# Kernel tuning notes

Hardware: AMD Instinct MI355X
Metric: run time of the kernel (lower is better)

Reference implementation:

```python
import jax, jax.numpy as jnp
import numpy as np

X = 512; Y = 512; C = 3; NK = 15
DT = 0.2; DD = 2; SIGMA = 0.95
THETA_X = 2.0; N_EXP = 2.0
K_SIZE = 16

# mesh-grid positions, cell centers at +0.5 (matches construct_mesh_grid)
POS = (jnp.stack(jnp.meshgrid(jnp.arange(X), jnp.arange(Y), indexing='ij'), axis=-1) + 0.5).astype(jnp.float32)  # [X,Y,2]


def _dwconv(img, k):
    # img [X,Y,C'] -> depthwise 3x3 cross-correlation with 'same' zero padding (matches torch conv2d)
    z = img.transpose(2, 0, 1)[None]                      # [1,C',X,Y]
    kern = jnp.tile(k[None, None], (z.shape[1], 1, 1, 1))  # [C',1,3,3]
    out = jax.lax.conv_general_dilated(z, kern, (1, 1), 'SAME', feature_group_count=z.shape[1])
    return out[0].transpose(1, 2, 0)


def _sobel(img):
    # returns [X,Y,2,C'] with (sy, sx) stacked on axis 2, matching torch code order
    kx = jnp.array([[-1., 0., 1.], [-2., 0., 2.], [-1., 0., 1.]], jnp.float32)
    return jnp.stack([_dwconv(img, kx.T), _dwconv(img, kx)], axis=2)


def _reintegrate(grid, F):
    # Flow-Lenia reintegration tracking: 25 static roll offsets, fused accumulation
    ma = DD - SIGMA
    mu = POS[..., None] + jnp.clip(DT * F, -ma, ma)  # [X,Y,2,C]
    mu = jnp.clip(mu, SIGMA, X - SIGMA)
    clip_hi = min(1.0, 2.0 * SIGMA)
    inv_area = 1.0 / (4.0 * SIGMA ** 2)
    acc = jnp.zeros_like(grid)
    for dx in range(-DD, DD + 1):
        for dy in range(-DD, DD + 1):
            gridR = jnp.roll(grid, (dx, dy), (0, 1))
            muR = jnp.roll(mu, (dx, dy), (0, 1))
            sz = 0.5 - jnp.abs(POS[..., None] - muR) + SIGMA
            area = jnp.prod(jnp.clip(sz, 0.0, clip_hi), axis=2) * inv_area  # [X,Y,C]
            acc = acc + gridR * area
    return acc


def _forward(x, Ks, m, s, h, w_c1, c0):
    # spectral kernels: normalize, fftshift, fft2 (matches construct_kernels)
    Ksn = Ks / Ks.sum(axis=(0, 1), keepdims=True)
    fk = jnp.fft.fft2(jnp.fft.fftshift(Ksn, axes=(0, 1)), axes=(0, 1))  # [X,Y,NK] complex
    fXs = jnp.fft.fft2(x, axes=(0, 1))
    Us = jnp.fft.ifft2(fk * fXs[:, :, c0], axes=(0, 1)).real            # [X,Y,NK]
    # growth * h (note: h appears again inside w_c1, faithful to original double multiply)
    Gs = (jnp.exp(-(((Us - m) / s) ** 2) * 0.5) * 2.0 - 1.0) * h
    Hs = jnp.einsum('xyk,kc->xyc', Gs, w_c1)                             # [X,Y,C]
    grad_u = _sobel(Hs)                                                  # [X,Y,2,C]
    grad_x = _sobel(x.sum(-1, keepdims=True))                            # [X,Y,2,1]
    alpha = jnp.clip((x[:, :, None, :] / THETA_X) ** N_EXP, 0.0, 1.0)    # [X,Y,1,C]
    F = grad_u * (1.0 - alpha) - grad_x * alpha                          # [X,Y,2,C]
    return _reintegrate(x, F)


def setup_inputs() -> dict:
    key = jax.random.key(0)
    k1, k2, k3, k4, k5 = jax.random.split(key, 5)
    x = jax.random.uniform(k1, (X, Y, C), jnp.float32)
    # ring kernels per construct_kernels (non-sparse branch)
    mg = np.mgrid[-X // 2:X // 2, -Y // 2:Y // 2]
    base = np.linalg.norm(mg, axis=0).astype(np.float32)
    ks_list = []
    for i in range(NK):
        r = 0.6 + 0.04 * i
        D = base / ((K_SIZE + 15) * r)
        sig = 0.5 * (np.tanh(-(D - 1.0) * 10.0 / 2.0) + 1.0)
        bell = np.exp(-(D - 0.5) ** 2 / 0.15)
        ks_list.append(sig * bell)
    Ks = jnp.asarray(np.stack(ks_list, -1).astype(np.float32))
    m = 0.1 + 0.3 * jax.random.uniform(k2, (NK,), jnp.float32)
    s = 0.03 + 0.15 * jax.random.uniform(k3, (NK,), jnp.float32)
    h = 0.3 + 0.7 * jax.random.uniform(k4, (NK,), jnp.float32)
    c0 = jax.random.randint(k5, (NK,), 0, C, jnp.int32)
    c1 = jnp.arange(NK) % C
    w_c1 = jax.nn.one_hot(c1, C, dtype=jnp.float32) * h[:, None]
    return {"x": x, "Ks": Ks, "m": m, "s": s, "h": h, "w_c1": w_c1, "c0": c0}


def reference(x, Ks, m, s, h, w_c1, c0):
    return _forward(x, Ks, m, s, h, w_c1, c0)
```

## Files before the change

### kernel.cpp

```cpp
#include <hip/hip_runtime.h>
#include <math.h>

#define NPIX 262144
#define NKER 15
#define PI_F 3.14159265358979323846f
#define HW 264
#define CS 578
#define SK(n) ((n) + ((n) >> 3))

__device__ __forceinline__ float2 cadd(float2 a, float2 b) { return make_float2(a.x + b.x, a.y + b.y); }
__device__ __forceinline__ float2 csub(float2 a, float2 b) { return make_float2(a.x - b.x, a.y - b.y); }
__device__ __forceinline__ float2 cmul(float2 a, float2 b) {
  return make_float2(a.x * b.x - a.y * b.y, a.x * b.y + a.y * b.x);
}

__device__ __forceinline__ void fft_roots(int lane, float2* w1, float2* wh) {
  float s, c;
  sincosf(-2.0f * PI_F * (float)lane / 512.0f, &s, &c);
  *w1 = make_float2(c, s);
  int h = lane & ~7;
  *wh = make_float2(__shfl(c, h, 64), __shfl(s, h, 64));
}

template <bool INV>
__device__ __forceinline__ void dft8(float2 a[8]) {
  const float R = 0.70710678118654752f;
  float2 t0 = cadd(a[0], a[4]), u0 = csub(a[0], a[4]);
  float2 t1 = cadd(a[1], a[5]), u1 = csub(a[1], a[5]);
  float2 t2 = cadd(a[2], a[6]), u2 = csub(a[2], a[6]);
  float2 t3 = cadd(a[3], a[7]), u3 = csub(a[3], a[7]);
  u1 = INV ? make_float2(R * (u1.x - u1.y), R * (u1.x + u1.y))
           : make_float2(R * (u1.x + u1.y), R * (u1.y - u1.x));
  u2 = INV ? make_float2(-u2.y, u2.x) : make_float2(u2.y, -u2.x);
  u3 = INV ? make_float2(-R * (u3.x + u3.y), R * (u3.x - u3.y))
           : make_float2(R * (u3.y - u3.x), -R * (u3.x + u3.y));
  float2 e0 = cadd(t0, t2), f0 = csub(t0, t2);
  float2 e1 = cadd(t1, t3), f1 = csub(t1, t3);
  f1 = INV ? make_float2(-f1.y, f1.x) : make_float2(f1.y, -f1.x);
  float2 g0 = cadd(u0, u2), h0 = csub(u0, u2);
  float2 g1 = cadd(u1, u3), h1 = csub(u1, u3);
  h1 = INV ? make_float2(-h1.y, h1.x) : make_float2(h1.y, -h1.x);
  a[0] = cadd(e0, e1); a[4] = csub(e0, e1);
  a[2] = cadd(f0, f1); a[6] = csub(f0, f1);
  a[1] = cadd(g0, g1); a[5] = csub(g0, g1);
  a[3] = cadd(h0, h1); a[7] = csub(h0, h1);
}

template <bool INV>
__device__ __forceinline__ void fft512_r8(float2 a[8], float2* buf, int lane,
                                          float2 w1, float2 wh) {
  float2 wa = INV ? make_float2(w1.x, -w1.y) : w1;
  float2 wb = INV ? make_float2(wh.x, -wh.y) : wh;
  dft8<INV>(a);
  {
    float2 tq = wa;
    a[1] = cmul(a[1], tq);
#pragma unroll
    for (int q = 2; q < 8; ++q) { tq = cmul(tq, wa); a[q] = cmul(a[q], tq); }
  }
#pragma unroll
  for (int q = 0; q < 8; ++q) buf[9 * lane + q] = a[q];
#pragma unroll
  for (int q = 0; q < 8; ++q) a[q] = buf[SK(lane + 64 * q)];
  dft8<INV>(a);
  {
    float2 tq = wb;
    a[1] = cmul(a[1], tq);
#pragma unroll
    for (int q = 2; q < 8; ++q) { tq = cmul(tq, wb); a[q] = cmul(a[q], tq); }
  }
  int h = lane & ~7;
  int b2 = 9 * h + (lane - h);
#pragma unroll
  for (int q = 0; q < 8; ++q) buf[b2 + 9 * q] = a[q];
#pragma unroll
  for (int q = 0; q < 8; ++q) a[q] = buf[SK(lane + 64 * q)];
  dft8<INV>(a);
}

__device__ __forceinline__ void split_store_halfplane(float2 a[8], float2* buf, int lane,
                                                      float2* d0, float2* d1) {
#pragma unroll
  for (int q = 0; q < 8; ++q) buf[SK(lane + 64 * q)] = a[q];
#pragma unroll
  for (int q = 0; q < 4; ++q) {
    int v = lane + 64 * q;
    int mir = (512 - v) & 511;
    float2 P = a[q];
    float2 Qc = buf[SK(mir)];
    float2 Q = make_float2(Qc.x, -Qc.y);
    d0[v] = make_float2(0.5f * (P.x + Q.x), 0.5f * (P.y + Q.y));
    d1[v] = make_float2(0.5f * (P.y - Q.y), -0.5f * (P.x - Q.x));
  }
  if (lane == 0) {
    float2 P = a[4];
    d0[256] = make_float2(P.x, 0.f);
    d1[256] = make_float2(P.y, 0.f);
  }
}

__global__ void prep_rows(const float* __restrict__ Ks, const float* __restrict__ x,
                          float* __restrict__ Kt, float* __restrict__ partial,
                          float2* __restrict__ AxH) {
  __shared__ float wsum[4][16];
  __shared__ float2 scr[4][CS];
  int t = threadIdx.x, wave = t >> 6, lane = t & 63;
  if (blockIdx.x < 1024) {
    int p = blockIdx.x * 256 + t;
    const float* src = Ks + (size_t)p * NKER;
    float v[NKER];
#pragma unroll
    for (int k = 0; k < NKER; ++k) v[k] = src[k];
#pragma unroll
    for (int k = 0; k < NKER; ++k) Kt[(size_t)k * NPIX + p] = v[k];
#pragma unroll
    for (int k = 0; k < NKER; ++k) {
#pragma unroll
      for (int off = 32; off > 0; off >>= 1) v[k] += __shfl_down(v[k], off, 64);
    }
    if ((t & 63) == 0) {
#pragma unroll
      for (int k = 0; k < NKER; ++k) wsum[wave][k] = v[k];
    }
    __syncthreads();
    if (t < NKER)
      partial[blockIdx.x * 16 + t] = wsum[0][t] + wsum[1][t] + wsum[2][t] + wsum[3][t];
  } else {
    int b = blockIdx.x - 1024;
    int c = b >> 6;
    int rp = (b & 63) * 4 + wave;
    int r0 = rp, r1 = rp + 256;
    float2 w1, wh;
    fft_roots(lane, &w1, &wh);
    float2 a[8];
#pragma unroll
    for (int q = 0; q < 8; ++q) {
      int y = lane + 64 * q;
      a[q] = make_float2(x[((size_t)r0 * 512 + y) * 3 + c],
                         x[((size_t)r1 * 512 + y) * 3 + c]);
    }
    fft512_r8<false>(a, &scr[wave][0], lane, w1, wh);
    float2* d0 = AxH + ((size_t)c * 512 + r0) * HW;
    float2* d1 = AxH + ((size_t)c * 512 + r1) * HW;
    split_store_halfplane(a, &scr[wave][0], lane, d0, d1);
  }
}

__global__ void fft_rows_k(const float* __restrict__ Kt, float2* __restrict__ AkH) {
  __shared__ float2 scr[4][CS];
  int t = threadIdx.x, wave = t >> 6, lane = t & 63;
  int rp = blockIdx.x * 4 + wave;
  int k = blockIdx.y;
  const float* s0 = Kt + (size_t)k * NPIX + (size_t)(rp + 256) * 512;
  const float* s1 = Kt + (size_t)k * NPIX + (size_t)rp * 512;
  float2 w1, wh;
  fft_roots(lane, &w1, &wh);
  float2 a[8];
#pragma unroll
  for (int q = 0; q < 8; ++q) {
    int ys = (lane + 64 * q + 256) & 511;
    a[q] = make_float2(s0[ys], s1[ys]);
  }
  fft512_r8<false>(a, &scr[wave][0], lane, w1, wh);
  float2* d0 = AkH + ((size_t)k * 512 + rp) * HW;
  float2* d1 = AkH + ((size_t)k * 512 + rp + 256) * HW;
  split_store_halfplane(a, &scr[wave][0], lane, d0, d1);
}

__global__ void cols_x(const float2* __restrict__ AxH, float2* __restrict__ XH,
                       const float* __restrict__ partial, float* __restrict__ sums) {
  __shared__ float2 buf[8 * CS];
  __shared__ float red[512];
  int t = threadIdx.x;
  if (blockIdx.x == 33) {
    if (blockIdx.y != 0) return;
    int k = t & 15, g = t >> 4;
    float acc = 0.f;
    for (int b = g; b < 1024; b += 32) acc += partial[b * 16 + k];
    red[t] = acc;
    __syncthreads();
    if (t < 16) {
      float s = 0.f;
#pragma unroll
      for (int g2 = 0; g2 < 32; ++g2) s += red[g2 * 16 + t];
      sums[t] = s;
    }
    return;
  }
  int col0 = blockIdx.x * 8, ch = blockIdx.y;
  int c = t >> 6, lane = t & 63;
  float2 w1, wh;
  fft_roots(lane, &w1, &wh);
  const float2* bx = AxH + (size_t)ch * 512 * HW;
  float2* dst = XH + (size_t)ch * 512 * HW;
#pragma unroll
  for (int u = 0; u < 8; ++u) {
    int idx = (u << 9) + t;
    int row = idx >> 3, cc = idx & 7;
    buf[cc * CS + SK(row)] = bx[(size_t)row * HW + col0 + cc];
  }
  __syncthreads();
  float2 a[8];
#pragma unroll
  for (int q = 0; q < 8; ++q) a[q] = buf[c * CS + SK(lane + 64 * q)];
  fft512_r8<false>(a, &buf[c * CS], lane, w1, wh);
#pragma unroll
  for (int q = 0; q < 8; ++q) buf[c * CS + SK(lane + 64 * q)] = a[q];
  __syncthreads();
#pragma unroll
  for (int u = 0; u < 8; ++u) {
    int idx = (u << 9) + t;
    int row = idx >> 3, cc = idx & 7;
    dst[(size_t)row * HW + col0 + cc] = buf[cc * CS + SK(row)];
  }
}

__global__ void fused_cols(float2* __restrict__ AkH, const float2* __restrict__ XH,
                           const int* __restrict__ c0) {
  __shared__ float2 buf[8 * CS];
  int t = threadIdx.x, col0 = blockIdx.x * 8, k = blockIdx.y;
  int c = t >> 6, lane = t & 63;
  float2 w1, wh;
  fft_roots(lane, &w1, &wh);
  const float2* bx = XH + (size_t)c0[k] * 512 * HW;
  float2* bk = AkH + (size_t)k * 512 * HW;
  int col = col0 + c;
  float2 xh[8];
#pragma unroll
  for (int q = 0; q < 8; ++q) xh[q] = bx[(size_t)(lane + 64 * q) * HW + col];
#pragma unroll
  for (int u = 0; u < 8; ++u) {
    int idx = (u << 9) + t;
    int row = idx >> 3, cc = idx & 7;
    buf[cc * CS + SK(row)] = bk[(size_t)row * HW + col0 + cc];
  }
  __syncthreads();
  float2 a[8];
#pragma unroll
  for (int q = 0; q < 8; ++q) a[q] = buf[c * CS + SK(lane + 64 * q)];
  fft512_r8<false>(a, &buf[c * CS], lane, w1, wh);
#pragma unroll
  for (int q = 0; q < 8; ++q) a[q] = cmul(a[q], xh[q]);
  fft512_r8<true>(a, &buf[c * CS], lane, w1, wh);
#pragma unroll
  for (int q = 0; q < 8; ++q) buf[c * CS + SK(lane + 64 * q)] = a[q];
  __syncthreads();
#pragma unroll
  for (int u = 0; u < 8; ++u) {
    int idx = (u << 9) + t;
    int row = idx >> 3, cc = idx & 7;
    bk[(size_t)row * HW + col0 + cc] = buf[cc * CS + SK(row)];
  }
}

__global__ void irows_growth_combine(const float2* __restrict__ AkH,
                                     const float* __restrict__ sums,
                                     const float* __restrict__ m, const float* __restrict__ s,
                                     const float* __restrict__ h, const float* __restrict__ w,
                                     float* __restrict__ Hs) {
  __shared__ float2 scr[4][CS];
  __shared__ float accL[4][3][512];
  __shared__ float mk[16], isk[16], hk[16], wk[16][3], sck[16];
  int t = threadIdx.x, wave = t >> 6, lane = t & 63;
  int row = blockIdx.x;
  if (t < NKER) {
    mk[t] = m[t]; isk[t] = 1.0f / s[t]; hk[t] = h[t];
    sck[t] = 1.0f / (sums[t] * 262144.0f);
    wk[t][0] = w[t * 3 + 0]; wk[t][1] = w[t * 3 + 1]; wk[t][2] = w[t * 3 + 2];
  }
  __syncthreads();
  float2 w1, wh;
  fft_roots(lane, &w1, &wh);
  float acc[3][8];
#pragma unroll
  for (int cc = 0; cc < 3; ++cc)
#pragma unroll
    for (int q = 0; q < 8; ++q) acc[cc][q] = 0.f;
  for (int si = 0; si < 2; ++si) {
    int slot = wave + 4 * si;
    int k1 = 2 * slot, k2 = 2 * slot + 1;
    bool dual = (k2 < NKER);
    const float2* p1 = AkH + ((size_t)k1 * 512 + row) * HW;
    const float2* p2 = AkH + ((size_t)(dual ? k2 : k1) * 512 + row) * HW;
    float2 a[8];
#pragma unroll
    for (int q = 0; q < 8; ++q) {
      int v = lane + 64 * q;
      if (v <= 256) {
        float2 A1 = p1[v];
        float2 A2 = dual ? p2[v] : make_float2(0.f, 0.f);
        a[q] = make_float2(A1.x - A2.y, A1.y + A2.x);
      } else {
        int mi = 512 - v;
        float2 A1 = p1[mi];
        float2 A2 = dual ? p2[mi] : make_float2(0.f, 0.f);
        a[q] = make_float2(A1.x + A2.y, -A1.y + A2.x);
      }
    }
    fft512_r8<true>(a, &scr[wave][0], lane, w1, wh);
    float m1 = mk[k1], i1 = isk[k1], h1 = hk[k1], s1 = sck[k1];
    float w10 = wk[k1][0], w11 = wk[k1][1], w12 = wk[k1][2];
#pragma unroll
    for (int q = 0; q < 8; ++q) {
      float tt = (a[q].x * s1 - m1) * i1;
      float g = (expf(-0.5f * tt * tt) * 2.0f - 1.0f) * h1;
      acc[0][q] += g * w10; acc[1][q] += g * w11; acc[2][q] += g * w12;
    }
    if (dual) {
      float m2 = mk[k2], i2 = isk[k2], h2 = hk[k2], s2 = sck[k2];
      float w20 = wk[k2][0], w21 = wk[k2][1], w22 = wk[k2][2];
#pragma unroll
      for (int q = 0; q < 8; ++q) {
        float tt = (a[q].y * s2 - m2) * i2;
        float g = (expf(-0.5f * tt * tt) * 2.0f - 1.0f) * h2;
        acc[0][q] += g * w20; acc[1][q] += g * w21; acc[2][q] += g * w22;
      }
    }
  }
#pragma unroll
  for (int cc = 0; cc < 3; ++cc)
#pragma unroll
    for (int q = 0; q < 8; ++q) accL[wave][cc][lane + 64 * q] = acc[cc][q];
  __syncthreads();
#pragma unroll
  for (int cc = 0; cc < 3; ++cc) {
#pragma unroll
    for (int rep = 0; rep < 2; ++rep) {
      int p = t + (rep << 8);
      float v = accL[0][cc][p] + accL[1][cc][p] + accL[2][cc][p] + accL[3][cc][p];
      Hs[(size_t)cc * NPIX + (size_t)row * 512 + p] = v;
    }
  }
}

__global__ void flow_reint(const float* __restrict__ x, const float* __restrict__ Hs,
                           float* __restrict__ out) {
  __shared__ float muT[20 * 20 * 6];
  __shared__ float xT[20 * 20 * 3];
  int ox = (blockIdx.x >> 5) << 4;
  int oy = (blockIdx.x & 31) << 4;
  for (int i = threadIdx.x; i < 400; i += 256) {
    int hi = i / 20, hj = i % 20;
    int qx = (ox - 2 + hi) & 511, qy = (oy - 2 + hj) & 511;
    float syH0 = 0.f, syH1 = 0.f, syH2 = 0.f;
    float sxH0 = 0.f, sxH1 = 0.f, sxH2 = 0.f;
    float syX = 0.f, sxX = 0.f;
#pragma unroll
    for (int di = -1; di <= 1; ++di) {
#pragma unroll
      for (int dj = -1; dj <= 1; ++dj) {
        if (di == 0 && dj == 0) continue;
        int xi = qx + di, yj = qy + dj;
        if ((unsigned)xi >= 512u || (unsigned)yj >= 512u) continue;
        float wy = (float)di * ((dj == 0) ? 2.f : 1.f);
        float wx = (float)dj * ((di == 0) ? 2.f : 1.f);
        int q = (xi << 9) | yj;
        float h0 = Hs[q], h1 = Hs[NPIX + q], h2 = Hs[2 * NPIX + q];
        syH0 += wy * h0; syH1 += wy * h1; syH2 += wy * h2;
        sxH0 += wx * h0; sxH1 += wx * h1; sxH2 += wx * h2;
        float xs = x[(size_t)q * 3 + 0] + x[(size_t)q * 3 + 1] + x[(size_t)q * 3 + 2];
        syX += wy * xs; sxX += wx * xs;
      }
    }
    int qp = (qx << 9) | qy;
    float cxq = (float)qx + 0.5f, cyq = (float)qy + 0.5f;
    float syH[3] = {syH0, syH1, syH2};
    float sxH[3] = {sxH0, sxH1, sxH2};
    int b6 = i * 6, b3 = i * 3;
#pragma unroll
    for (int c = 0; c < 3; ++c) {
      float xc = x[(size_t)qp * 3 + c];
      xT[b3 + c] = xc;
      float tt = xc * 0.5f;
      float alpha = fminf(tt * tt, 1.0f);
      float F0 = syH[c] * (1.f - alpha) - syX * alpha;
      float F1 = sxH[c] * (1.f - alpha) - sxX * alpha;
      float m0 = cxq + fminf(fmaxf(0.2f * F0, -1.05f), 1.05f);
      float m1 = cyq + fminf(fmaxf(0.2f * F1, -1.05f), 1.05f);
      muT[b6 + c]     = fminf(fmaxf(m0, 0.95f), 511.05f);
      muT[b6 + 3 + c] = fminf(fmaxf(m1, 0.95f), 511.05f);
    }
  }
  __syncthreads();
  int o = threadIdx.x;
  int lx = o >> 4, ly = o & 15;
  int px_ = ox + lx, py_ = oy + ly;
  float cx = (float)px_ + 0.5f, cy = (float)py_ + 0.5f;
  float a0 = 0.f, a1 = 0.f, a2 = 0.f;
#pragma unroll
  for (int dx = -2; dx <= 2; ++dx) {
    int hi = lx + 2 - dx;
#pragma unroll
    for (int dy = -2; dy <= 2; ++dy) {
      int hj = ly + 2 - dy;
      int b6 = (hi * 20 + hj) * 6, b3 = (hi * 20 + hj) * 3;
      float wv;
      wv = fminf(fmaxf(1.45f - fabsf(cx - muT[b6 + 0]), 0.f), 1.f) *
           fminf(fmaxf(1.45f - fabsf(cy - muT[b6 + 3]), 0.f), 1.f);
      a0 += xT[b3 + 0] * wv;
      wv = fminf(fmaxf(1.45f - fabsf(cx - muT[b6 + 1]), 0.f), 1.f) *
           fminf(fmaxf(1.45f - fabsf(cy - muT[b6 + 4]), 0.f), 1.f);
      a1 += xT[b3 + 1] * wv;
      wv = fminf(fmaxf(1.45f - fabsf(cx - muT[b6 + 2]), 0.f), 1.f) *
           fminf(fmaxf(1.45f - fabsf(cy - muT[b6 + 5]), 0.f), 1.f);
      a2 += xT[b3 + 2] * wv;
    }
  }
  const float inv_area = 0.27700831f;
  size_t p = (size_t)((px_ << 9) | py_);
  out[p * 3 + 0] = a0 * inv_area;
  out[p * 3 + 1] = a1 * inv_area;
  out[p * 3 + 2] = a2 * inv_area;
}

extern "C" void kernel_launch(void* const* d_in, const int* in_sizes, int n_in,
                              void* d_out, int out_size, void* d_ws, size_t ws_size,
                              hipStream_t stream) {
  const float* x    = (const float*)d_in[0];
  const float* Ks   = (const float*)d_in[1];
  const float* m    = (const float*)d_in[2];
  const float* s    = (const float*)d_in[3];
  const float* h    = (const float*)d_in[4];
  const float* w_c1 = (const float*)d_in[5];
  const int*   c0   = (const int*)d_in[6];
  float* out = (float*)d_out;

  char* ws = (char*)d_ws;
  size_t off = 0;
  float* sums    = (float*)(ws + off); off += 1024;
  float* partial = (float*)(ws + off); off += 1024 * 16 * 4;
  float*  Kt   = (float*)(ws + off);  off += (size_t)NKER * NPIX * 4;
  float2* AxH  = (float2*)(ws + off); off += (size_t)3 * 512 * HW * 8;
  float2* XH   = (float2*)(ws + off); off += (size_t)3 * 512 * HW * 8;
  float2* AkH  = (float2*)(ws + off); off += (size_t)NKER * 512 * HW * 8;
  float*  Hs   = (float*)(ws + off);  off += (size_t)3 * NPIX * 4;

  prep_rows<<<1216, 256, 0, stream>>>(Ks, x, Kt, partial, AxH);
  fft_rows_k<<<dim3(64, NKER), 256, 0, stream>>>(Kt, AkH);
  cols_x<<<dim3(34, 3), 512, 0, stream>>>(AxH, XH, partial, sums);
  fused_cols<<<dim3(33, NKER), 512, 0, stream>>>(AkH, XH, c0);
  irows_growth_combine<<<512, 256, 0, stream>>>(AkH, sums, m, s, h, w_c1, Hs);
  flow_reint<<<1024, 256, 0, stream>>>(x, Hs, out);
}
```

Baseline: 147.7 us.

## Fuse kernel transpose into row FFTs and store column FFT of x transposed

Removes the separate Ks transpose pass (Kt buffer) by loading each Ks row into shared memory and performing row FFTs on pairs of kernels directly, with partial sums computed in the same block. The x column FFT now writes its output column-major (XHt) so fused_cols reads contiguous columns instead of strided rows, and one launch is eliminated. The change cuts a full write and reread of the kernel stack. It relies on large shared memory per block (krow is 30KB) and pairs kernel k with k+1, so one slot writes into an extra 16th AkH plane.

```diff
diff --git a/kernel.cpp b/kernel.cpp
--- a/kernel.cpp
+++ b/kernel.cpp
@@ -5,6 +5,7 @@
 #define NKER 15
 #define PI_F 3.14159265358979323846f
 #define HW 264
+#define NCOL 264
 #define CS 578
 #define SK(n) ((n) + ((n) >> 3))
 
@@ -99,39 +100,60 @@
   }
 }
 
-__global__ void prep_rows(const float* __restrict__ Ks, const float* __restrict__ x,
-                          float* __restrict__ Kt, float* __restrict__ partial,
-                          float2* __restrict__ AxH) {
-  __shared__ float wsum[4][16];
+__global__ void rows_all(const float* __restrict__ Ks, const float* __restrict__ x,
+                         float* __restrict__ partial, float2* __restrict__ AkH,
+                         float2* __restrict__ AxH) {
+  __shared__ float krow[512 * NKER];
   __shared__ float2 scr[4][CS];
+  __shared__ float psum[480];
   int t = threadIdx.x, wave = t >> 6, lane = t & 63;
-  if (blockIdx.x < 1024) {
-    int p = blockIdx.x * 256 + t;
-    const float* src = Ks + (size_t)p * NKER;
-    float v[NKER];
-#pragma unroll
-    for (int k = 0; k < NKER; ++k) v[k] = src[k];
-#pragma unroll
-    for (int k = 0; k < NKER; ++k) Kt[(size_t)k * NPIX + p] = v[k];
-#pragma unroll
-    for (int k = 0; k < NKER; ++k) {
-#pragma unroll
-      for (int off = 32; off > 0; off >>= 1) v[k] += __shfl_down(v[k], off, 64);
-    }
-    if ((t & 63) == 0) {
-#pragma unroll
-      for (int k = 0; k < NKER; ++k) wsum[wave][k] = v[k];
-    }
+  float2 w1, wh;
+  fft_roots(lane, &w1, &wh);
+  if (blockIdx.x < 512) {
+    int b = blockIdx.x;
+    int rs = (b + 256) & 511;
+    const float2* src = (const float2*)Ks + (size_t)rs * 3840;
+    float2* kr2 = (float2*)krow;
+#pragma unroll
+    for (int i = 0; i < 15; ++i) kr2[t + 256 * i] = src[t + 256 * i];
     __syncthreads();
-    if (t < NKER)
-      partial[blockIdx.x * 16 + t] = wsum[0][t] + wsum[1][t] + wsum[2][t] + wsum[3][t];
+    for (int i = t; i < 480; i += 256) {
+      int k = i >> 5, yg = i & 31;
+      float s = 0.f;
+      int base = yg * 16;
+#pragma unroll
+      for (int y = 0; y < 16; ++y) s += krow[(base + y) * NKER + k];
+      psum[i] = s;
+    }
+#pragma unroll
+    for (int si = 0; si < 2; ++si) {
+      int slot = wave + 4 * si;
+      int k1 = 2 * slot, k2 = k1 + 1;
+      float2 a[8];
+#pragma unroll
+      for (int q = 0; q < 8; ++q) {
+        int ys = (lane + 64 * q + 256) & 511;
+        float re = krow[ys * NKER + k1];
+        float im = (k2 < NKER) ? krow[ys * NKER + k2] : 0.f;
+        a[q] = make_float2(re, im);
+      }
+      fft512_r8<false>(a, &scr[wave][0], lane, w1, wh);
+      float2* d0 = AkH + ((size_t)k1 * 512 + b) * HW;
+      float2* d1 = AkH + ((size_t)k2 * 512 + b) * HW;
+      split_store_halfplane(a, &scr[wave][0], lane, d0, d1);
+    }
+    __syncthreads();
+    if (t < NKER) {
+      float s = 0.f;
+#pragma unroll
+      for (int g = 0; g < 32; ++g) s += psum[(t << 5) + g];
+      partial[b * 16 + t] = s;
+    }
   } else {
-    int b = blockIdx.x - 1024;
+    int b = blockIdx.x - 512;
     int c = b >> 6;
     int rp = (b & 63) * 4 + wave;
     int r0 = rp, r1 = rp + 256;
-    float2 w1, wh;
-    fft_roots(lane, &w1, &wh);
     float2 a[8];
 #pragma unroll
     for (int q = 0; q < 8; ++q) {
@@ -146,37 +168,15 @@
   }
 }
 
-__global__ void fft_rows_k(const float* __restrict__ Kt, float2* __restrict__ AkH) {
-  __shared__ float2 scr[4][CS];
-  int t = threadIdx.x, wave = t >> 6, lane = t & 63;
-  int rp = blockIdx.x * 4 + wave;
-  int k = blockIdx.y;
-  const float* s0 = Kt + (size_t)k * NPIX + (size_t)(rp + 256) * 512;
-  const float* s1 = Kt + (size_t)k * NPIX + (size_t)rp * 512;
-  float2 w1, wh;
-  fft_roots(lane, &w1, &wh);
-  float2 a[8];
-#pragma unroll
-  for (int q = 0; q < 8; ++q) {
-    int ys = (lane + 64 * q + 256) & 511;
-    a[q] = make_float2(s0[ys], s1[ys]);
-  }
-  fft512_r8<false>(a, &scr[wave][0], lane, w1, wh);
-  float2* d0 = AkH + ((size_t)k * 512 + rp) * HW;
-  float2* d1 = AkH + ((size_t)k * 512 + rp + 256) * HW;
-  split_store_halfplane(a, &scr[wave][0], lane, d0, d1);
-}
-
-__global__ void cols_x(const float2* __restrict__ AxH, float2* __restrict__ XH,
-                       const float* __restrict__ partial, float* __restrict__ sums) {
+__global__ void mid_cols(const float2* __restrict__ AxH, float2* __restrict__ XHt,
+                         const float* __restrict__ partial, float* __restrict__ sums) {
   __shared__ float2 buf[8 * CS];
   __shared__ float red[512];
   int t = threadIdx.x;
-  if (blockIdx.x == 33) {
-    if (blockIdx.y != 0) return;
+  if (blockIdx.x == 99) {
     int k = t & 15, g = t >> 4;
     float acc = 0.f;
-    for (int b = g; b < 1024; b += 32) acc += partial[b * 16 + k];
+    for (int b = g; b < 512; b += 32) acc += partial[b * 16 + k];
     red[t] = acc;
     __syncthreads();
     if (t < 16) {
@@ -187,12 +187,12 @@
     }
     return;
   }
-  int col0 = blockIdx.x * 8, ch = blockIdx.y;
+  int ch = blockIdx.x / 33, slab = blockIdx.x % 33;
+  int col0 = slab * 8;
   int c = t >> 6, lane = t & 63;
   float2 w1, wh;
   fft_roots(lane, &w1, &wh);
   const float2* bx = AxH + (size_t)ch * 512 * HW;
-  float2* dst = XH + (size_t)ch * 512 * HW;
 #pragma unroll
   for (int u = 0; u < 8; ++u) {
     int idx = (u << 9) + t;
@@ -204,30 +204,23 @@
 #pragma unroll
   for (int q = 0; q < 8; ++q) a[q] = buf[c * CS + SK(lane + 64 * q)];
   fft512_r8<false>(a, &buf[c * CS], lane, w1, wh);
-#pragma unroll
-  for (int q = 0; q < 8; ++q) buf[c * CS + SK(lane + 64 * q)] = a[q];
-  __syncthreads();
-#pragma unroll
-  for (int u = 0; u < 8; ++u) {
-    int idx = (u << 9) + t;
-    int row = idx >> 3, cc = idx & 7;
-    dst[(size_t)row * HW + col0 + cc] = buf[cc * CS + SK(row)];
-  }
-}
-
-__global__ void fused_cols(float2* __restrict__ AkH, const float2* __restrict__ XH,
+  float2* dst = XHt + ((size_t)ch * NCOL + col0 + c) * 512;
+#pragma unroll
+  for (int q = 0; q < 8; ++q) dst[lane + 64 * q] = a[q];
+}
+
+__global__ void fused_cols(float2* __restrict__ AkH, const float2* __restrict__ XHt,
                            const int* __restrict__ c0) {
   __shared__ float2 buf[8 * CS];
   int t = threadIdx.x, col0 = blockIdx.x * 8, k = blockIdx.y;
   int c = t >> 6, lane = t & 63;
   float2 w1, wh;
   fft_roots(lane, &w1, &wh);
-  const float2* bx = XH + (size_t)c0[k] * 512 * HW;
   float2* bk = AkH + (size_t)k * 512 * HW;
-  int col = col0 + c;
+  const float2* xcol = XHt + ((size_t)c0[k] * NCOL + col0 + c) * 512;
   float2 xh[8];
 #pragma unroll
-  for (int q = 0; q < 8; ++q) xh[q] = bx[(size_t)(lane + 64 * q) * HW + col];
+  for (int q = 0; q < 8; ++q) xh[q] = xcol[lane + 64 * q];
 #pragma unroll
   for (int u = 0; u < 8; ++u) {
     int idx = (u << 9) + t;
@@ -428,17 +421,15 @@
   char* ws = (char*)d_ws;
   size_t off = 0;
   float* sums    = (float*)(ws + off); off += 1024;
-  float* partial = (float*)(ws + off); off += 1024 * 16 * 4;
-  float*  Kt   = (float*)(ws + off);  off += (size_t)NKER * NPIX * 4;
+  float* partial = (float*)(ws + off); off += 512 * 16 * 4;
   float2* AxH  = (float2*)(ws + off); off += (size_t)3 * 512 * HW * 8;
-  float2* XH   = (float2*)(ws + off); off += (size_t)3 * 512 * HW * 8;
-  float2* AkH  = (float2*)(ws + off); off += (size_t)NKER * 512 * HW * 8;
+  float2* XHt  = (float2*)(ws + off); off += (size_t)3 * NCOL * 512 * 8;
+  float2* AkH  = (float2*)(ws + off); off += (size_t)16 * 512 * HW * 8;
   float*  Hs   = (float*)(ws + off);  off += (size_t)3 * NPIX * 4;
 
-  prep_rows<<<1216, 256, 0, stream>>>(Ks, x, Kt, partial, AxH);
-  fft_rows_k<<<dim3(64, NKER), 256, 0, stream>>>(Kt, AkH);
-  cols_x<<<dim3(34, 3), 512, 0, stream>>>(AxH, XH, partial, sums);
-  fused_cols<<<dim3(33, NKER), 512, 0, stream>>>(AkH, XH, c0);
+  rows_all<<<704, 256, 0, stream>>>(Ks, x, partial, AkH, AxH);
+  mid_cols<<<100, 512, 0, stream>>>(AxH, XHt, partial, sums);
+  fused_cols<<<dim3(33, NKER), 512, 0, stream>>>(AkH, XHt, c0);
   irows_growth_combine<<<512, 256, 0, stream>>>(AkH, sums, m, s, h, w_c1, Hs);
   flow_reint<<<1024, 256, 0, stream>>>(x, Hs, out);
 }
```

New measurement: 135.4 us. 8.3% less time.
